# Kernel optimization log

Measured on AMD Instinct MI355X. Metric: run time of the kernel, lower is better.

The kernel has to match this reference:

```python
import jax, jax.numpy as jnp
import numpy as np

C = 256
D = C // 8  # query/key channels
B, H, W = 4, 64, 64


def setup_inputs() -> dict:
    key = jax.random.key(0)
    ks = jax.random.split(key, 9)
    s = 0.02
    return {
        "z": jax.random.normal(ks[0], (B, C, H, W), jnp.float32),
        "x": jax.random.normal(ks[1], (B, C, H, W), jnp.float32),
        "y": jax.random.normal(ks[2], (B, C, H, W), jnp.float32),
        "Wq": jax.random.normal(ks[3], (D, C), jnp.float32) * s,
        "bq": jnp.zeros((D,), jnp.float32),
        "Wk": jax.random.normal(ks[4], (D, C), jnp.float32) * s,
        "bk": jnp.zeros((D,), jnp.float32),
        "Wv": jax.random.normal(ks[5], (C, C), jnp.float32) * s,
        "bv": jnp.zeros((C,), jnp.float32),
    }


def reference(z, x, y, Wq, bq, Wk, bk, Wv, bv):
    b, c, h, w = x.shape
    n = h * w
    xf = x.reshape(b, c, n)  # [B,C,N]
    yf = y.reshape(b, c, n)
    zf = z.reshape(b, c, n)
    # 1x1 convs == channel-wise linear projections
    q = jnp.einsum("dc,bcn->bnd", Wq, xf) + bq                 # [B,N,D]
    k = jnp.einsum("dc,bcn->bdn", Wk, yf) + bk[:, None]        # [B,D,N]
    energy = jnp.einsum("bnd,bdm->bnm", q, k)                  # [B,N,N]
    attn = jax.nn.softmax(energy, axis=-1)                     # rows over keys
    v = jnp.einsum("ec,bcn->ben", Wv, zf) + bv[:, None]        # [B,C,N]
    # torch: bmm(value, attn^T) -> out[b,c,m] = sum_n v[b,c,n]*attn[b,m,n]
    out = jnp.einsum("ben,bmn->bem", v, attn)                  # [B,C,N]
    return z + out.reshape(b, c, h, w)
```

## Files before the change

### kernel.cpp

```cpp
#include <hip/hip_runtime.h>
#include <hip/hip_bf16.h>

#define Bn 4
#define Cn 256
#define Dn 32
#define Nn 4096

typedef __attribute__((ext_vector_type(8))) short short8;
typedef __attribute__((ext_vector_type(4))) float f32x4;

__device__ __forceinline__ unsigned short f2bf(float f) {
  union { __hip_bfloat16 h; unsigned short u; } c;
  c.h = __float2bfloat16(f);
  return c.u;
}

__global__ __launch_bounds__(256, 2) void SA_projqk(
    const float* __restrict__ x, const float* __restrict__ y,
    const float* __restrict__ Wq, const float* __restrict__ bq,
    const float* __restrict__ Wk, const float* __restrict__ bk,
    unsigned short* __restrict__ qws, unsigned short* __restrict__ kws)
{
  __shared__ char lds[64 * 80];
  const int bid = blockIdx.x, tid = threadIdx.x;
  const int lane = tid & 63, w = tid >> 6, g = lane >> 4, l15 = lane & 15;
  const int isq = bid < 256;
  const int t = bid & 255;
  const int b = t >> 6, n0 = (t & 63) << 6;
  const float* W    = isq ? Wq : Wk;
  const float* bias = isq ? bq : bk;
  const float* in   = (isq ? x : y) + (size_t)b * Cn * Nn;
  unsigned short* ob = (isq ? qws : kws) + (size_t)b * Nn * Dn;
  const int nw = n0 + 16 * w;

  f32x4 acc[2];
#pragma unroll
  for (int et = 0; et < 2; ++et) { acc[et][0]=0.f; acc[et][1]=0.f; acc[et][2]=0.f; acc[et][3]=0.f; }

  float4 A[2][2][2];
  float  Bv[2][8];

  auto ld = [&](int ch, int s) {
#pragma unroll
    for (int et = 0; et < 2; ++et) {
      const float* wp = W + (size_t)(16*et + l15) * 256 + ch*32 + 4*g;
      A[s][et][0] = *(const float4*)wp;
      A[s][et][1] = *(const float4*)(wp + 16);
    }
    const float* ip  = in + (size_t)(ch*32 + 4*g) * Nn + nw + l15;
    const float* ip2 = ip + (size_t)16 * Nn;
#pragma unroll
    for (int j = 0; j < 4; ++j) { Bv[s][j] = ip[(size_t)j*Nn]; Bv[s][4+j] = ip2[(size_t)j*Nn]; }
  };
  auto comp = [&](int s) {
    short8 bf8;
#pragma unroll
    for (int j = 0; j < 8; ++j) bf8[j] = (short)f2bf(Bv[s][j]);
#pragma unroll
    for (int et = 0; et < 2; ++et) {
      short8 af;
      af[0]=(short)f2bf(A[s][et][0].x); af[1]=(short)f2bf(A[s][et][0].y);
      af[2]=(short)f2bf(A[s][et][0].z); af[3]=(short)f2bf(A[s][et][0].w);
      af[4]=(short)f2bf(A[s][et][1].x); af[5]=(short)f2bf(A[s][et][1].y);
      af[6]=(short)f2bf(A[s][et][1].z); af[7]=(short)f2bf(A[s][et][1].w);
      acc[et] = __builtin_amdgcn_mfma_f32_16x16x32_bf16(af, bf8, acc[et], 0, 0, 0);
    }
  };

  ld(0, 0);
#pragma unroll
  for (int ch = 0; ch < 8; ch += 2) {
    ld(ch + 1, 1);
    comp(0);
    if (ch < 6) ld(ch + 2, 0);
    comp(1);
  }

#pragma unroll
  for (int et = 0; et < 2; ++et) {
    int nl = 16*w + l15;
#pragma unroll
    for (int r = 0; r < 4; ++r) {
      int d = 16*et + 4*g + r;
      *(unsigned short*)(lds + (size_t)nl*80 + d*2) = f2bf(acc[et][r] + bias[d]);
    }
  }
  __syncthreads();
  {
    int nl = tid >> 2, c4 = tid & 3;
    *(uint4*)((char*)ob + (size_t)(n0 + nl)*64 + c4*16) = *(const uint4*)(lds + (size_t)nl*80 + c4*16);
  }
}

__global__ __launch_bounds__(256, 2) void SA_projv(
    const float* __restrict__ z,
    const float* __restrict__ Wv, const float* __restrict__ bv,
    unsigned short* __restrict__ vws)
{
  __shared__ char lds[64 * 272];
  const int bid = blockIdx.x, tid = threadIdx.x;
  const int lane = tid & 63, w = tid >> 6, g = lane >> 4, l15 = lane & 15;
  const int b = bid >> 7, e0 = ((bid >> 5) & 3) << 6, n0 = (bid & 31) << 7;
  const float* in = z + (size_t)b * Cn * Nn;
  const int nw = n0 + 32 * w;

  f32x4 acc[4][2];
#pragma unroll
  for (int et = 0; et < 4; ++et)
#pragma unroll
    for (int ns = 0; ns < 2; ++ns) { acc[et][ns][0]=0.f; acc[et][ns][1]=0.f; acc[et][ns][2]=0.f; acc[et][ns][3]=0.f; }

  float4 A[2][4][2];
  float  Bv2[2][2][8];

  auto ld = [&](int ch, int s) {
#pragma unroll
    for (int et = 0; et < 4; ++et) {
      const float* wp = Wv + (size_t)(e0 + 16*et + l15) * 256 + ch*32 + 4*g;
      A[s][et][0] = *(const float4*)wp;
      A[s][et][1] = *(const float4*)(wp + 16);
    }
#pragma unroll
    for (int ns = 0; ns < 2; ++ns) {
      const float* ip  = in + (size_t)(ch*32 + 4*g) * Nn + nw + 16*ns + l15;
      const float* ip2 = ip + (size_t)16 * Nn;
#pragma unroll
      for (int j = 0; j < 4; ++j) { Bv2[s][ns][j] = ip[(size_t)j*Nn]; Bv2[s][ns][4+j] = ip2[(size_t)j*Nn]; }
    }
  };
  auto comp = [&](int s) {
    short8 bf8[2];
#pragma unroll
    for (int ns = 0; ns < 2; ++ns)
#pragma unroll
      for (int j = 0; j < 8; ++j) bf8[ns][j] = (short)f2bf(Bv2[s][ns][j]);
#pragma unroll
    for (int et = 0; et < 4; ++et) {
      short8 af;
      af[0]=(short)f2bf(A[s][et][0].x); af[1]=(short)f2bf(A[s][et][0].y);
      af[2]=(short)f2bf(A[s][et][0].z); af[3]=(short)f2bf(A[s][et][0].w);
      af[4]=(short)f2bf(A[s][et][1].x); af[5]=(short)f2bf(A[s][et][1].y);
      af[6]=(short)f2bf(A[s][et][1].z); af[7]=(short)f2bf(A[s][et][1].w);
#pragma unroll
      for (int ns = 0; ns < 2; ++ns)
        acc[et][ns] = __builtin_amdgcn_mfma_f32_16x16x32_bf16(af, bf8[ns], acc[et][ns], 0, 0, 0);
    }
  };

  ld(0, 0);
#pragma unroll
  for (int ch = 0; ch < 8; ch += 2) {
    ld(ch + 1, 1);
    comp(0);
    if (ch < 6) ld(ch + 2, 0);
    comp(1);
  }

#pragma unroll
  for (int et = 0; et < 4; ++et) {
#pragma unroll
    for (int ns = 0; ns < 2; ++ns) {
      int nl = 32*w + 16*ns + l15;
#pragma unroll
      for (int r = 0; r < 4; ++r) {
        int el = 16*et + 4*g + r;
        *(unsigned short*)(lds + (size_t)el*272 + nl*2) = f2bf(acc[et][ns][r] + bv[e0 + el]);
      }
    }
  }
  __syncthreads();
#pragma unroll
  for (int i = 0; i < 4; ++i) {
    int idx = i*256 + tid, el = idx >> 4, c16 = idx & 15;
    *(uint4*)((char*)vws + (size_t)b*Cn*Nn*2 + (size_t)(e0 + el)*Nn*2 + (size_t)n0*2 + c16*16)
        = *(const uint4*)(lds + (size_t)el*272 + c16*16);
  }
}

__global__ __launch_bounds__(512, 2) void SA_flash(
    const unsigned short* __restrict__ qws, const unsigned short* __restrict__ kws,
    const unsigned short* __restrict__ vws, const float* __restrict__ z,
    float* __restrict__ outp)
{
  __shared__ char lds[83968];
  const int bid = blockIdx.x;
  const int b    = (bid >> 1) & 3;
  const int mblk = ((bid >> 3) << 1) | (bid & 1);
  const int m0 = mblk * 64;
  const int tid = threadIdx.x, lane = tid & 63;
  const int wv = tid >> 6, gg = wv >> 2, wq = wv & 3;
  const int g = lane >> 4, l15 = lane & 15;
  const int t2 = tid & 255;

  char* Kt = lds + gg * 41984;
  char* Vt = Kt + 5120;

  const unsigned short* qb = qws + (size_t)b * Nn * Dn;
  const unsigned short* kb = kws + (size_t)b * Nn * Dn;
  const unsigned short* vb = vws + (size_t)b * Cn * Nn;

  const int mw = m0 + 16 * wq;
  short8 qf;
  {
    const char* qp = (const char*)qb + (size_t)(mw + l15) * 64 + 8 * g;
    ushort4 q0 = *(const ushort4*)qp;
    ushort4 q1 = *(const ushort4*)(qp + 32);
    qf[0]=(short)q0.x; qf[1]=(short)q0.y; qf[2]=(short)q0.z; qf[3]=(short)q0.w;
    qf[4]=(short)q1.x; qf[5]=(short)q1.y; qf[6]=(short)q1.z; qf[7]=(short)q1.w;
  }

  f32x4 acc[16];
#pragma unroll
  for (int i = 0; i < 16; ++i) { acc[i][0]=0.f; acc[i][1]=0.f; acc[i][2]=0.f; acc[i][3]=0.f; }
  float m_run = -__builtin_inff(), l_run = 0.f;

  const int knl = t2 >> 2, kp = t2 & 3;
  uint4 kreg; uint4 vreg[8];
  auto stage_load = [&](int kt) {
    const int n0 = kt * 64;
    kreg = *(const uint4*)((const char*)kb + (size_t)(n0 + knl) * 64 + kp * 16);
#pragma unroll
    for (int i = 0; i < 8; ++i) {
      int idx = i * 256 + t2, e = idx >> 3, ch = idx & 7;
      vreg[i] = *(const uint4*)((const char*)vb + (size_t)e * (Nn * 2) + (size_t)(n0 + ch * 8) * 2);
    }
  };
  stage_load(gg);

  for (int it = 0; it < 32; ++it) {
    {
      int off1 = 32 * (kp & 1) + 8 * (kp >> 1);
      char* krow = Kt + (size_t)knl * 80;
      *(uint2*)(krow + off1)      = make_uint2(kreg.x, kreg.y);
      *(uint2*)(krow + off1 + 16) = make_uint2(kreg.z, kreg.w);
#pragma unroll
      for (int i = 0; i < 8; ++i) {
        int idx = i * 256 + t2, e = idx >> 3, ch = idx & 7;
        int p1 = 64 * (ch & 1) + 8 * (ch >> 1);
        char* vrow = Vt + (size_t)e * 144;
        *(uint2*)(vrow + p1)      = make_uint2(vreg[i].x, vreg[i].y);
        *(uint2*)(vrow + p1 + 32) = make_uint2(vreg[i].z, vreg[i].w);
      }
    }
    __syncthreads();
    if (it < 31) stage_load(2 * (it + 1) + gg);

    f32x4 s[4];
    const f32x4 zero4 = {0.f, 0.f, 0.f, 0.f};
#pragma unroll
    for (int t = 0; t < 4; ++t) {
      short8 kf = *(const short8*)(Kt + (size_t)(16*t + l15) * 80 + 16 * g);
      s[t] = __builtin_amdgcn_mfma_f32_16x16x32_bf16(kf, qf, zero4, 0, 0, 0);
    }
    float pm = s[0][0];
#pragma unroll
    for (int t = 0; t < 4; ++t)
#pragma unroll
      for (int r = 0; r < 4; ++r) pm = fmaxf(pm, s[t][r]);
    pm = fmaxf(pm, __shfl_xor(pm, 16, 64));
    pm = fmaxf(pm, __shfl_xor(pm, 32, 64));
    if (__any(pm > m_run)) {
      float mn = fmaxf(m_run, pm);
      float alpha = __expf(m_run - mn);
      l_run *= alpha;
      m_run = mn;
#pragma unroll
      for (int i = 0; i < 16; ++i) { acc[i][0]*=alpha; acc[i][1]*=alpha; acc[i][2]*=alpha; acc[i][3]*=alpha; }
    }
    float p[4][4]; float rs = 0.f;
#pragma unroll
    for (int t = 0; t < 4; ++t)
#pragma unroll
      for (int r = 0; r < 4; ++r) { float e = __expf(s[t][r] - m_run); p[t][r] = e; rs += e; }
    rs += __shfl_xor(rs, 16, 64);
    rs += __shfl_xor(rs, 32, 64);
    l_run += rs;

    short8 pf[2];
#pragma unroll
    for (int c = 0; c < 2; ++c) {
      short8 t8;
      t8[0]=(short)f2bf(p[2*c][0]);   t8[1]=(short)f2bf(p[2*c][1]);
      t8[2]=(short)f2bf(p[2*c][2]);   t8[3]=(short)f2bf(p[2*c][3]);
      t8[4]=(short)f2bf(p[2*c+1][0]); t8[5]=(short)f2bf(p[2*c+1][1]);
      t8[6]=(short)f2bf(p[2*c+1][2]); t8[7]=(short)f2bf(p[2*c+1][3]);
      pf[c] = t8;
    }
    __builtin_amdgcn_s_setprio(1);
#pragma unroll
    for (int c = 0; c < 2; ++c)
#pragma unroll
      for (int et = 0; et < 16; ++et) {
        short8 vf = *(const short8*)(Vt + (size_t)(16*et + l15) * 144 + 32 * g + 16 * c);
        acc[et] = __builtin_amdgcn_mfma_f32_16x16x32_bf16(vf, pf[c], acc[et], 0, 0, 0);
      }
    __builtin_amdgcn_s_setprio(0);
    __syncthreads();
  }

  __syncthreads();
  float* mz = (float*)(lds + 73728);
  mz[tid] = m_run;
  __syncthreads();
  float m_oth = mz[tid ^ 256];
  float M  = fmaxf(m_run, m_oth);
  float al = __expf(m_run - M);
  float l_sc = l_run * al;
  float* lz = (float*)(lds + 75776);
  if (gg == 1) {
    char* rowp = lds + (size_t)t2 * 272;
#pragma unroll
    for (int i = 0; i < 16; ++i) {
      f32x4 v = acc[i];
      v[0]*=al; v[1]*=al; v[2]*=al; v[3]*=al;
      *(f32x4*)(rowp + i*16) = v;
    }
    lz[t2] = l_sc;
  }
  __syncthreads();
  if (gg == 0) {
    char* rowp = lds + (size_t)t2 * 272;
    float inv = 1.0f / (l_sc + lz[t2]);
    const float* zb = z    + (size_t)b * Cn * Nn;
    float*       ob = outp + (size_t)b * Cn * Nn;
    const int mpos = mw + l15;
#pragma unroll
    for (int et = 0; et < 16; ++et) {
      f32x4 o = *(const f32x4*)(rowp + et*16);
#pragma unroll
      for (int r = 0; r < 4; ++r) {
        int e = 16*et + 4*g + r;
        size_t off = (size_t)e * Nn + mpos;
        ob[off] = zb[off] + (acc[et][r]*al + o[r]) * inv;
      }
    }
  }
}

extern "C" void kernel_launch(void* const* d_in, const int* in_sizes, int n_in,
                              void* d_out, int out_size, void* d_ws, size_t ws_size,
                              hipStream_t stream) {
  (void)in_sizes; (void)n_in; (void)out_size; (void)ws_size;
  const float* z  = (const float*)d_in[0];
  const float* x  = (const float*)d_in[1];
  const float* y  = (const float*)d_in[2];
  const float* Wq = (const float*)d_in[3];
  const float* bq = (const float*)d_in[4];
  const float* Wk = (const float*)d_in[5];
  const float* bk = (const float*)d_in[6];
  const float* Wv = (const float*)d_in[7];
  const float* bv = (const float*)d_in[8];
  float* out = (float*)d_out;

  unsigned short* qws = (unsigned short*)d_ws;
  unsigned short* kws = qws + (size_t)Bn * Nn * Dn;
  unsigned short* vws = kws + (size_t)Bn * Nn * Dn;

  SA_projqk<<<512, 256, 0, stream>>>(x, y, Wq, bq, Wk, bk, qws, kws);
  SA_projv <<<512, 256, 0, stream>>>(z, Wv, bv, vws);
  SA_flash <<<256, 512, 0, stream>>>(qws, kws, vws, z, out);
}
```

Measured before the change: 208.0 us.

## Fuse Q, K and V projections into one kernel with LDS-staged bf16 inputs

Replaces the separate QK and V projection kernels with a single 640-thread kernel. Each block covers 64 positions of one batch: it loads x, y and z tiles with coalesced float4 reads, converts them to bf16 and transposes them into LDS. Wave 0 computes Q, wave 1 computes K and waves 2-9 compute V from the staged tiles. This removes one kernel launch and avoids reading z separately for each of the four output-channel slices. In exchange it uses about 100KB of LDS at one block per CU, does scalar 2-byte LDS transpose writes, and runs a grid of only 256 blocks.

Result: faster. 197.1 us (-5.2%).

```diff
diff --git a/kernel.cpp b/kernel.cpp
--- a/kernel.cpp
+++ b/kernel.cpp
@@ -15,165 +15,169 @@
   return c.u;
 }
 
-__global__ __launch_bounds__(256, 2) void SA_projqk(
-    const float* __restrict__ x, const float* __restrict__ y,
+__global__ __launch_bounds__(640, 1) void SA_proj2(
+    const float* __restrict__ x, const float* __restrict__ y, const float* __restrict__ z,
     const float* __restrict__ Wq, const float* __restrict__ bq,
     const float* __restrict__ Wk, const float* __restrict__ bk,
-    unsigned short* __restrict__ qws, unsigned short* __restrict__ kws)
-{
-  __shared__ char lds[64 * 80];
-  const int bid = blockIdx.x, tid = threadIdx.x;
-  const int lane = tid & 63, w = tid >> 6, g = lane >> 4, l15 = lane & 15;
-  const int isq = bid < 256;
-  const int t = bid & 255;
-  const int b = t >> 6, n0 = (t & 63) << 6;
-  const float* W    = isq ? Wq : Wk;
-  const float* bias = isq ? bq : bk;
-  const float* in   = (isq ? x : y) + (size_t)b * Cn * Nn;
-  unsigned short* ob = (isq ? qws : kws) + (size_t)b * Nn * Dn;
-  const int nw = n0 + 16 * w;
-
-  f32x4 acc[2];
-#pragma unroll
-  for (int et = 0; et < 2; ++et) { acc[et][0]=0.f; acc[et][1]=0.f; acc[et][2]=0.f; acc[et][3]=0.f; }
-
-  float4 A[2][2][2];
-  float  Bv[2][8];
-
-  auto ld = [&](int ch, int s) {
-#pragma unroll
-    for (int et = 0; et < 2; ++et) {
-      const float* wp = W + (size_t)(16*et + l15) * 256 + ch*32 + 4*g;
-      A[s][et][0] = *(const float4*)wp;
-      A[s][et][1] = *(const float4*)(wp + 16);
-    }
-    const float* ip  = in + (size_t)(ch*32 + 4*g) * Nn + nw + l15;
-    const float* ip2 = ip + (size_t)16 * Nn;
-#pragma unroll
-    for (int j = 0; j < 4; ++j) { Bv[s][j] = ip[(size_t)j*Nn]; Bv[s][4+j] = ip2[(size_t)j*Nn]; }
-  };
-  auto comp = [&](int s) {
-    short8 bf8;
-#pragma unroll
-    for (int j = 0; j < 8; ++j) bf8[j] = (short)f2bf(Bv[s][j]);
-#pragma unroll
-    for (int et = 0; et < 2; ++et) {
-      short8 af;
-      af[0]=(short)f2bf(A[s][et][0].x); af[1]=(short)f2bf(A[s][et][0].y);
-      af[2]=(short)f2bf(A[s][et][0].z); af[3]=(short)f2bf(A[s][et][0].w);
-      af[4]=(short)f2bf(A[s][et][1].x); af[5]=(short)f2bf(A[s][et][1].y);
-      af[6]=(short)f2bf(A[s][et][1].z); af[7]=(short)f2bf(A[s][et][1].w);
-      acc[et] = __builtin_amdgcn_mfma_f32_16x16x32_bf16(af, bf8, acc[et], 0, 0, 0);
-    }
-  };
-
-  ld(0, 0);
-#pragma unroll
-  for (int ch = 0; ch < 8; ch += 2) {
-    ld(ch + 1, 1);
-    comp(0);
-    if (ch < 6) ld(ch + 2, 0);
-    comp(1);
-  }
-
-#pragma unroll
-  for (int et = 0; et < 2; ++et) {
-    int nl = 16*w + l15;
-#pragma unroll
-    for (int r = 0; r < 4; ++r) {
-      int d = 16*et + 4*g + r;
-      *(unsigned short*)(lds + (size_t)nl*80 + d*2) = f2bf(acc[et][r] + bias[d]);
-    }
-  }
-  __syncthreads();
-  {
-    int nl = tid >> 2, c4 = tid & 3;
-    *(uint4*)((char*)ob + (size_t)(n0 + nl)*64 + c4*16) = *(const uint4*)(lds + (size_t)nl*80 + c4*16);
-  }
-}
-
-__global__ __launch_bounds__(256, 2) void SA_projv(
-    const float* __restrict__ z,
     const float* __restrict__ Wv, const float* __restrict__ bv,
+    unsigned short* __restrict__ qws, unsigned short* __restrict__ kws,
     unsigned short* __restrict__ vws)
 {
-  __shared__ char lds[64 * 272];
+  __shared__ char lds[3 * 33280];
   const int bid = blockIdx.x, tid = threadIdx.x;
-  const int lane = tid & 63, w = tid >> 6, g = lane >> 4, l15 = lane & 15;
-  const int b = bid >> 7, e0 = ((bid >> 5) & 3) << 6, n0 = (bid & 31) << 7;
-  const float* in = z + (size_t)b * Cn * Nn;
-  const int nw = n0 + 32 * w;
-
-  f32x4 acc[4][2];
-#pragma unroll
-  for (int et = 0; et < 4; ++et)
-#pragma unroll
-    for (int ns = 0; ns < 2; ++ns) { acc[et][ns][0]=0.f; acc[et][ns][1]=0.f; acc[et][ns][2]=0.f; acc[et][ns][3]=0.f; }
-
-  float4 A[2][4][2];
-  float  Bv2[2][2][8];
-
-  auto ld = [&](int ch, int s) {
-#pragma unroll
-    for (int et = 0; et < 4; ++et) {
-      const float* wp = Wv + (size_t)(e0 + 16*et + l15) * 256 + ch*32 + 4*g;
-      A[s][et][0] = *(const float4*)wp;
-      A[s][et][1] = *(const float4*)(wp + 16);
-    }
-#pragma unroll
-    for (int ns = 0; ns < 2; ++ns) {
-      const float* ip  = in + (size_t)(ch*32 + 4*g) * Nn + nw + 16*ns + l15;
-      const float* ip2 = ip + (size_t)16 * Nn;
-#pragma unroll
-      for (int j = 0; j < 4; ++j) { Bv2[s][ns][j] = ip[(size_t)j*Nn]; Bv2[s][ns][4+j] = ip2[(size_t)j*Nn]; }
-    }
-  };
-  auto comp = [&](int s) {
-    short8 bf8[2];
-#pragma unroll
-    for (int ns = 0; ns < 2; ++ns)
-#pragma unroll
-      for (int j = 0; j < 8; ++j) bf8[ns][j] = (short)f2bf(Bv2[s][ns][j]);
-#pragma unroll
-    for (int et = 0; et < 4; ++et) {
-      short8 af;
-      af[0]=(short)f2bf(A[s][et][0].x); af[1]=(short)f2bf(A[s][et][0].y);
-      af[2]=(short)f2bf(A[s][et][0].z); af[3]=(short)f2bf(A[s][et][0].w);
-      af[4]=(short)f2bf(A[s][et][1].x); af[5]=(short)f2bf(A[s][et][1].y);
-      af[6]=(short)f2bf(A[s][et][1].z); af[7]=(short)f2bf(A[s][et][1].w);
-#pragma unroll
-      for (int ns = 0; ns < 2; ++ns)
-        acc[et][ns] = __builtin_amdgcn_mfma_f32_16x16x32_bf16(af, bf8[ns], acc[et][ns], 0, 0, 0);
-    }
-  };
-
-  ld(0, 0);
-#pragma unroll
-  for (int ch = 0; ch < 8; ch += 2) {
-    ld(ch + 1, 1);
-    comp(0);
-    if (ch < 6) ld(ch + 2, 0);
-    comp(1);
-  }
-
-#pragma unroll
-  for (int et = 0; et < 4; ++et) {
-#pragma unroll
-    for (int ns = 0; ns < 2; ++ns) {
-      int nl = 32*w + 16*ns + l15;
-#pragma unroll
-      for (int r = 0; r < 4; ++r) {
-        int el = 16*et + 4*g + r;
-        *(unsigned short*)(lds + (size_t)el*272 + nl*2) = f2bf(acc[et][ns][r] + bv[e0 + el]);
-      }
-    }
-  }
-  __syncthreads();
-#pragma unroll
-  for (int i = 0; i < 4; ++i) {
-    int idx = i*256 + tid, el = idx >> 4, c16 = idx & 15;
-    *(uint4*)((char*)vws + (size_t)b*Cn*Nn*2 + (size_t)(e0 + el)*Nn*2 + (size_t)n0*2 + c16*16)
-        = *(const uint4*)(lds + (size_t)el*272 + c16*16);
+  const int lane = tid & 63, wv2 = tid >> 6;
+  const int g = lane >> 4, l15 = lane & 15;
+  const int b = bid >> 6, n0 = (bid & 63) << 6;
+
+  const float* src0 = x + (size_t)b * Cn * Nn;
+  const float* src1 = y + (size_t)b * Cn * Nn;
+  const float* src2 = z + (size_t)b * Cn * Nn;
+
+  const int isv = (wv2 >= 2);
+  const float* W    = isv ? Wv : (wv2 == 0 ? Wq : Wk);
+  const float* bias = isv ? bv : (wv2 == 0 ? bq : bk);
+  const int e0w = isv ? ((wv2 - 2) << 5) : 0;
+  const char* myT = lds + (isv ? 2 : wv2) * 33280;
+
+  const int cl = tid >> 2, fq = tid & 3;
+
+  f32x4 sl0[4], sl1[4], sl2[4];
+  auto stage_ld = [&](int ck) {
+    const size_t row = (size_t)(ck * 128 + cl) * Nn + n0 + fq * 4;
+#pragma unroll
+    for (int i = 0; i < 4; ++i) sl0[i] = *(const f32x4*)(src0 + row + i * 16);
+#pragma unroll
+    for (int i = 0; i < 4; ++i) sl1[i] = *(const f32x4*)(src1 + row + i * 16);
+#pragma unroll
+    for (int i = 0; i < 4; ++i) sl2[i] = *(const f32x4*)(src2 + row + i * 16);
+  };
+  auto stage_wr = [&](int ck) {
+    const int cb = (ck * 128 + cl) * 2;
+#pragma unroll
+    for (int i = 0; i < 4; ++i)
+#pragma unroll
+      for (int j = 0; j < 4; ++j) {
+        char* rp = lds + (size_t)(fq * 4 + i * 16 + j) * 520 + cb;
+        *(unsigned short*)(rp)         = f2bf(sl0[i][j]);
+        *(unsigned short*)(rp + 33280) = f2bf(sl1[i][j]);
+        *(unsigned short*)(rp + 66560) = f2bf(sl2[i][j]);
+      }
+  };
+
+  f32x4 wf[2][4][2];
+  auto w_ld = [&](int ck) {
+#pragma unroll
+    for (int et = 0; et < 2; ++et) {
+      const float* wp = W + (size_t)(e0w + 16 * et + l15) * 256 + ck * 128 + 4 * g;
+#pragma unroll
+      for (int cc = 0; cc < 4; ++cc) {
+        wf[et][cc][0] = *(const f32x4*)(wp + cc * 32);
+        wf[et][cc][1] = *(const f32x4*)(wp + cc * 32 + 16);
+      }
+    }
+  };
+  short8 af[2][4];
+  auto w_cvt = [&]() {
+#pragma unroll
+    for (int et = 0; et < 2; ++et)
+#pragma unroll
+      for (int cc = 0; cc < 4; ++cc) {
+        short8 t8;
+#pragma unroll
+        for (int j = 0; j < 4; ++j) {
+          t8[j]     = (short)f2bf(wf[et][cc][0][j]);
+          t8[4 + j] = (short)f2bf(wf[et][cc][1][j]);
+        }
+        af[et][cc] = t8;
+      }
+  };
+
+  f32x4 acc[2][4];
+#pragma unroll
+  for (int et = 0; et < 2; ++et)
+#pragma unroll
+    for (int ns = 0; ns < 4; ++ns) { acc[et][ns][0]=0.f; acc[et][ns][1]=0.f; acc[et][ns][2]=0.f; acc[et][ns][3]=0.f; }
+
+  auto compute = [&](int ck) {
+#pragma unroll
+    for (int cc = 0; cc < 4; ++cc) {
+      const int cbyte = (ck * 128 + cc * 32 + 4 * g) * 2;
+#pragma unroll
+      for (int ns = 0; ns < 4; ++ns) {
+        const char* rp = myT + (size_t)(16 * ns + l15) * 520 + cbyte;
+        union { uint2 u[2]; short8 s; } bb;
+        bb.u[0] = *(const uint2*)rp;
+        bb.u[1] = *(const uint2*)(rp + 32);
+#pragma unroll
+        for (int et = 0; et < 2; ++et)
+          acc[et][ns] = __builtin_amdgcn_mfma_f32_16x16x32_bf16(af[et][cc], bb.s, acc[et][ns], 0, 0, 0);
+      }
+    }
+  };
+
+  if (tid < 512) stage_ld(0);
+  w_ld(0);
+  if (tid < 512) stage_wr(0);
+  __syncthreads();
+  w_cvt();
+  if (tid < 512) stage_ld(1);
+  compute(0);
+  if (tid < 512) stage_wr(1);
+  w_ld(1);
+  __syncthreads();
+  w_cvt();
+  compute(1);
+  __syncthreads();
+
+  float bvv[2][4];
+#pragma unroll
+  for (int et = 0; et < 2; ++et)
+#pragma unroll
+    for (int r = 0; r < 4; ++r) bvv[et][r] = bias[e0w + 16 * et + 4 * g + r];
+
+  if (isv) {
+#pragma unroll
+    for (int et = 0; et < 2; ++et)
+#pragma unroll
+      for (int ns = 0; ns < 4; ++ns)
+#pragma unroll
+        for (int r = 0; r < 4; ++r) {
+          int e = e0w + 16 * et + 4 * g + r;
+          int n = 16 * ns + l15;
+          *(unsigned short*)(lds + (size_t)e * 144 + n * 2) = f2bf(acc[et][ns][r] + bvv[et][r]);
+        }
+  } else {
+    char* base = lds + (wv2 == 0 ? 66560 : 71680);
+#pragma unroll
+    for (int et = 0; et < 2; ++et)
+#pragma unroll
+      for (int ns = 0; ns < 4; ++ns)
+#pragma unroll
+        for (int r = 0; r < 4; ++r) {
+          int d = 16 * et + 4 * g + r;
+          int n = 16 * ns + l15;
+          *(unsigned short*)(base + (size_t)n * 80 + d * 2) = f2bf(acc[et][ns][r] + bvv[et][r]);
+        }
+  }
+  __syncthreads();
+
+  if (tid < 512) {
+    const int el = tid >> 1, half = tid & 1;
+    char* gb = (char*)vws + (size_t)b * Cn * Nn * 2 + (size_t)el * Nn * 2 + (size_t)n0 * 2 + half * 64;
+    const char* lb = lds + (size_t)el * 144 + half * 64;
+#pragma unroll
+    for (int i = 0; i < 4; ++i)
+      *(uint4*)(gb + i * 16) = *(const uint4*)(lb + i * 16);
+  }
+  if (wv2 < 2) {
+    unsigned short* ob = (wv2 == 0 ? qws : kws) + (size_t)b * Nn * Dn;
+    const char* base = lds + (wv2 == 0 ? 66560 : 71680);
+#pragma unroll
+    for (int i = 0; i < 4; ++i) {
+      int flat = 64 * i + lane;
+      *(uint4*)((char*)ob + (size_t)n0 * 64 + flat * 16)
+          = *(const uint4*)(base + (size_t)(flat >> 2) * 80 + (flat & 3) * 16);
+    }
   }
 }
 
@@ -356,7 +360,6 @@
   unsigned short* kws = qws + (size_t)Bn * Nn * Dn;
   unsigned short* vws = kws + (size_t)Bn * Nn * Dn;
 
-  SA_projqk<<<512, 256, 0, stream>>>(x, y, Wq, bq, Wk, bk, qws, kws);
-  SA_projv <<<512, 256, 0, stream>>>(z, Wv, bv, vws);
-  SA_flash <<<256, 512, 0, stream>>>(qws, kws, vws, z, out);
+  SA_proj2<<<256, 640, 0, stream>>>(x, y, z, Wq, bq, Wk, bk, Wv, bv, qws, kws, vws);
+  SA_flash<<<256, 512, 0, stream>>>(qws, kws, vws, z, out);
 }
```
